# Optimization experiments

Measured on AMD Instinct MI355X. Metric: run time of the kernel, lower is better.

The kernel has to match this reference:

```python
import jax, jax.numpy as jnp
import numpy as np

# dims: S samples, J u-functions, D outputs, P input dims, N data points
S, J, D, P, N = 8, 4, 4, 3, 1024
BG, BU, MG, MU = 32, 32, 10, 32  # g-RFF, u-RFF, g-inducing, u-inducing


def setup_inputs() -> dict:
    key = jax.random.key(0)
    ks = jax.random.split(key, 16)
    ts = jax.random.normal(ks[0], (N, P), dtype=jnp.float32)
    alphas = jax.random.uniform(ks[1], (D, P), minval=0.5, maxval=1.5)   # filter window precisions
    pgs = jax.random.uniform(ks[2], (D, P), minval=0.5, maxval=1.5)      # g kernel precisions (ls2pr)
    zgs = jnp.tile(jnp.linspace(-1.0, 1.0, MG, dtype=jnp.float32)[:, None], (1, P))  # g inducing inputs
    thetag = 2.0 * jax.random.normal(ks[3], (D, P, BG))                  # g spectral freqs
    betag = jax.random.uniform(ks[4], (S, D, P, BG), minval=0.0, maxval=2 * np.pi)
    wg = jax.random.normal(ks[5], (S, D, P, BG)) / np.sqrt(BG)           # g RFF weights
    qg = 0.1 * jax.random.normal(ks[6], (S, D, P, MG))                   # g canonical weights (compute_q)
    pus = jax.random.uniform(ks[7], (P,), minval=0.5, maxval=1.5)        # u cross-kernel precisions
    zus = jax.random.normal(ks[8], (MU, P))                              # u inducing inputs
    thetau = 2.0 * jax.random.normal(ks[9], (S, J, P, BU))               # u spectral freqs
    betau = jax.random.uniform(ks[10], (S, J, BU), minval=0.0, maxval=2 * np.pi)
    wu = jax.random.normal(ks[11], (S, J, BU)) / np.sqrt(BU)
    qu = 0.1 * jax.random.normal(ks[12], (S, J, MU))                     # u canonical weights
    ampu = jnp.float32(1.0)
    log_amps = 0.1 * jax.random.normal(ks[13], (D, J))
    W = jax.random.normal(ks[14], (P, D)) / np.sqrt(P)
    return dict(ts=ts, alphas=alphas, pgs=pgs, zgs=zgs, thetag=thetag, betag=betag,
                wg=wg, qg=qg, pus=pus, zus=zus, thetau=thetau, betau=betau,
                wu=wu, qu=qu, ampu=ampu, log_amps=log_amps, W=W)


def reference(ts, alphas, pgs, zgs, thetag, betag, wg, qg, pus, zus,
              thetau, betau, wu, qu, ampu, log_amps, W):
    """NPGPLayer.forward: f_d(t) = sum_j amps[d,j] * I_dj(t) + ts @ W, where
    I_dj(t) = ampu * int_{R^P} [prod_p exp(-alpha_dp tau_p^2) g_dp(tau_p)] u_j(t - tau) dtau,
    with g, u sampled via random-Fourier + canonical (inducing) features; all 1-D
    Gaussian x cosine integrals are closed-form (this is the math of integrals.full_I)."""
    pi = jnp.pi
    amps = jnp.exp(log_amps)  # [D,J]

    # ---------- Part A: u RFF terms.  Fourier transform of windowed g at om ----------
    om = thetau  # [S,J,P,BU]
    aE = alphas[None, None, :, :, None, None]            # [1,1,D,P,1,1]
    th = thetag[None, None, :, :, None, :]               # [1,1,D,P,1,BG]
    omE = om[:, :, None, :, :, None]                     # [S,J,1,P,BU,1]
    e1 = jnp.exp(-(th - omE) ** 2 / (4 * aE))
    e2 = jnp.exp(-(th + omE) ** 2 / (4 * aE))
    cb = jnp.cos(betag)[:, None, :, :, None, :]
    sb = jnp.sin(betag)[:, None, :, :, None, :]
    wgE = wg[:, None, :, :, None, :]
    # int exp(-a tau^2) cos(th tau + b) e^{-i om tau} dtau
    Ghat_rff = jnp.sum(0.5 * jnp.sqrt(pi / aE) * wgE * ((e1 + e2) * cb + 1j * (e1 - e2) * sb), axis=-1)  # [S,J,D,P,BU]

    A = alphas + pgs                                     # [D,P]
    zT = zgs.T                                           # [P,MG]
    mu = pgs[:, :, None] * zT[None] / A[:, :, None]      # [D,P,MG]
    rg = alphas[:, :, None] * pgs[:, :, None] * zT[None] ** 2 / A[:, :, None]
    decay = jnp.exp(-om[:, :, None, :, :] ** 2 / (4 * A[None, None, :, :, None]))        # [S,J,D,P,BU]
    phase_mu = jnp.exp(-1j * om[:, :, None, :, :, None] * mu[None, None, :, :, None, :])  # [S,J,D,P,BU,MG]
    can_coef = jnp.sqrt(pi / A)[..., None] * jnp.exp(-rg)                                 # [D,P,MG]
    Ghat_can = jnp.sum(qg[:, None, :, :, None, :] * can_coef[None, None, :, :, None, :] * phase_mu, axis=-1) * decay
    Ghat = Ghat_rff + Ghat_can                           # [S,J,D,P,BU] complex

    phase_t = jnp.exp(1j * om[..., None] * ts.T[None, None, :, None, :])  # [S,J,P,BU,N]
    combined = Ghat[..., None] * phase_t[:, :, None]     # [S,J,D,P,BU,N]
    prodp = jnp.prod(combined, axis=3)                   # [S,J,D,BU,N]  (product over input dims)
    cu = wu * jnp.exp(1j * betau)                        # [S,J,BU]
    F_rff = jnp.real(jnp.einsum('sjb,sjdbn->sjdn', cu, prodp))

    # ---------- Part B: u canonical (inducing) terms -- Gaussian x Gaussian integrals ----------
    c = jnp.transpose(ts[:, None, :] - zus[None, :, :], (2, 0, 1))  # [P,N,MU]
    Bm = alphas + pus[None, :]                           # [D,P]
    mp = pus[None, :, None, None] * c[None] / Bm[:, :, None, None]                 # [D,P,N,MU]
    rp = alphas[:, :, None, None] * pus[None, :, None, None] * c[None] ** 2 / Bm[:, :, None, None]
    spec = jnp.sqrt(pi / Bm)[:, :, None] * jnp.exp(-thetag ** 2 / (4 * Bm[:, :, None]))  # [D,P,BG]
    arg = thetag[:, :, None, None, :] * mp[..., None]    # [D,P,N,MU,BG]
    cosx, sinx = jnp.cos(arg), jnp.sin(arg)
    coef1 = wg * jnp.cos(betag) * spec[None]             # [S,D,P,BG]
    coef2 = wg * jnp.sin(betag) * spec[None]
    term_rff = (jnp.einsum('dpnmb,sdpb->sdpnm', cosx, coef1)
                - jnp.einsum('dpnmb,sdpb->sdpnm', sinx, coef2)) * jnp.exp(-rp)[None]
    Cm = Bm + pgs                                        # [D,P]
    diff = mp[..., None] - zT[None, :, None, None, :]    # [D,P,N,MU,MG]
    r2 = Bm[:, :, None, None, None] * pgs[:, :, None, None, None] * diff ** 2 / Cm[:, :, None, None, None]
    val = jnp.sqrt(pi / Cm)[:, :, None, None, None] * jnp.exp(-rp[..., None] - r2)
    term_can = jnp.einsum('dpnmg,sdpg->sdpnm', val, qg)
    Gg = term_rff + term_can                             # [S,D,P,N,MU]
    prodg = jnp.prod(Gg, axis=2)                         # [S,D,N,MU]
    F_can = jnp.einsum('sjm,sdnm->sjdn', qu, prodg)

    F = ampu * (F_rff + F_can)                           # [S,J,D,N]
    layer = jnp.einsum('dj,sjdn->snd', amps, F)          # amps-weighted sum over u functions
    return layer + ts @ W                                # residual connection (is_final_layer=False)
```

## Files before the change

kernel.cpp:

```cpp
#include <hip/hip_runtime.h>
#include <math.h>

#define S_ 8
#define J_ 4
#define D_ 4
#define P_ 3
#define N_ 1024
#define BG_ 32
#define BU_ 32
#define MG_ 10
#define MU_ 32

static constexpr float PI_F = 3.14159265358979323846f;

#define COEF_OFF    0
#define CANPART_OFF 8192

#define NB_CAN  1024
#define NB_COEF 64

__global__ __launch_bounds__(256, 4) void fused_kernel(
    const float* __restrict__ ts,     const float* __restrict__ alphas,
    const float* __restrict__ pgs,    const float* __restrict__ zgs,
    const float* __restrict__ thetag, const float* __restrict__ betag,
    const float* __restrict__ wg,     const float* __restrict__ qg,
    const float* __restrict__ pus,    const float* __restrict__ zus,
    const float* __restrict__ thetau, const float* __restrict__ betau,
    const float* __restrict__ wu,     const float* __restrict__ qu,
    const float* __restrict__ ampu_p, const float* __restrict__ log_amps,
    float* __restrict__ ws)
{
    int bid = blockIdx.x;
    int t   = threadIdx.x;
    float ampu = ampu_p[0];

    if (bid < NB_CAN) {
        __shared__ float sc1[P_][BG_][S_];
        __shared__ float sc2[P_][BG_][S_];
        __shared__ float sqg[P_][MG_][S_];
        __shared__ float stg[P_][BG_];
        __shared__ float szg[P_][MG_];
        __shared__ float szu[P_][MU_];
        __shared__ float sts[4][P_];
        __shared__ float squ[S_][MU_];
        __shared__ float skmp[P_], skrp[P_], sksc[P_], skbc[P_];

        int d  = bid >> 8;
        int n0 = (bid & 255) * 4;

        for (int i = t; i < P_*BG_*S_; i += 256) {
            int p = i >> 8, b = (i >> 3) & 31, s = i & 7;
            float alpha = alphas[d*P_ + p];
            float Bm = alpha + pus[p];
            float th = thetag[(d*P_ + p)*BG_ + b];
            float spec = sqrtf(PI_F / Bm) * __expf(-th*th*0.25f/Bm);
            float be = betag[((s*D_ + d)*P_ + p)*BG_ + b];
            float w  = wg   [((s*D_ + d)*P_ + p)*BG_ + b];
            float sb, cb; __sincosf(be, &sb, &cb);
            sc1[p][b][s] = w * cb * spec;
            sc2[p][b][s] = w * sb * spec;
        }
        for (int i = t; i < P_*MG_*S_; i += 256) {
            int p = i / (MG_*S_), r = i % (MG_*S_), g = r >> 3, s = r & 7;
            ((float*)sqg)[i] = qg[((s*D_ + d)*P_ + p)*MG_ + g];
        }
        {
            int s = t >> 5, m = t & 31;
            float acc = 0.f;
            #pragma unroll
            for (int j = 0; j < J_; ++j)
                acc += __expf(log_amps[d*J_ + j]) * qu[(s*J_ + j)*MU_ + m];
            squ[s][m] = ampu * acc;
        }
        if (t < P_*BG_) ((float*)stg)[t] = thetag[d*P_*BG_ + t];
        if (t < P_*MG_) { int p = t / MG_, g = t % MG_; szg[p][g] = zgs[g*P_ + p]; }
        if (t >= 128 && t < 128 + P_*MU_) {
            int i = t - 128; int p = i >> 5, m = i & 31;
            szu[p][m] = zus[m*P_ + p];
        }
        if (t >= 96 && t < 96 + 4*P_) { int i = t - 96; sts[i/3][i%3] = ts[n0*P_ + i]; }
        if (t >= 112 && t < 112 + P_) {
            int p = t - 112;
            float alpha = alphas[d*P_ + p], pg = pgs[d*P_ + p], pu = pus[p];
            float Bm = alpha + pu, invB = 1.f / Bm;
            skmp[p] = pu * invB;
            skrp[p] = alpha * pu * invB;
            float Cm = Bm + pg, invC = 1.f / Cm;
            sksc[p] = sqrtf(PI_F * invC);
            skbc[p] = Bm * pg * invC;
        }
        __syncthreads();

        int m = t & 31, q = (t >> 5) & 1, nl = t >> 6;

        float pr0=1.f,pr1=1.f,pr2=1.f,pr3=1.f,pr4=1.f,pr5=1.f,pr6=1.f,pr7=1.f;

        #pragma unroll 1
        for (int p = 0; p < P_; ++p) {
            float c  = sts[nl][p] - szu[p][m];
            float mp = skmp[p] * c;
            float E  = __expf(-skrp[p] * c * c);
            float a0=0.f,a1=0.f,a2=0.f,a3=0.f,a4=0.f,a5=0.f,a6=0.f,a7=0.f;
            int b0 = q * 16;
            #pragma unroll 4
            for (int bb = 0; bb < 16; ++bb) {
                int b = b0 + bb;
                float sx, cx; __sincosf(stg[p][b] * mp, &sx, &cx);
                const float4* c1v = (const float4*)&sc1[p][b][0];
                const float4* c2v = (const float4*)&sc2[p][b][0];
                float4 u0 = c1v[0], u1 = c1v[1];
                float4 v0 = c2v[0], v1 = c2v[1];
                a0 += u0.x*cx - v0.x*sx;  a1 += u0.y*cx - v0.y*sx;
                a2 += u0.z*cx - v0.z*sx;  a3 += u0.w*cx - v0.w*sx;
                a4 += u1.x*cx - v1.x*sx;  a5 += u1.y*cx - v1.y*sx;
                a6 += u1.z*cx - v1.z*sx;  a7 += u1.w*cx - v1.w*sx;
            }
            int g0 = q * 5;
            #pragma unroll 1
            for (int gg = 0; gg < 5; ++gg) {
                int g = g0 + gg;
                float diff = mp - szg[p][g];
                float v = sksc[p] * __expf(-skbc[p]*diff*diff);
                const float4* qv = (const float4*)&sqg[p][g][0];
                float4 q0 = qv[0], q1 = qv[1];
                a0 += q0.x*v; a1 += q0.y*v; a2 += q0.z*v; a3 += q0.w*v;
                a4 += q1.x*v; a5 += q1.y*v; a6 += q1.z*v; a7 += q1.w*v;
            }
            a0 += __shfl_xor(a0, 32, 64); a1 += __shfl_xor(a1, 32, 64);
            a2 += __shfl_xor(a2, 32, 64); a3 += __shfl_xor(a3, 32, 64);
            a4 += __shfl_xor(a4, 32, 64); a5 += __shfl_xor(a5, 32, 64);
            a6 += __shfl_xor(a6, 32, 64); a7 += __shfl_xor(a7, 32, 64);
            pr0 *= E*a0; pr1 *= E*a1; pr2 *= E*a2; pr3 *= E*a3;
            pr4 *= E*a4; pr5 *= E*a5; pr6 *= E*a6; pr7 *= E*a7;
        }

        int n = n0 + nl;
        float prod[S_] = {pr0,pr1,pr2,pr3,pr4,pr5,pr6,pr7};
        int s0 = q * 4;
        #pragma unroll
        for (int ss = 0; ss < 4; ++ss) {
            int s = s0 + ss;
            float val = squ[s][m] * prod[s];
            #pragma unroll
            for (int off = 16; off; off >>= 1) val += __shfl_xor(val, off, 32);
            if (m == 0) ws[CANPART_OFF + (s*N_ + n)*D_ + d] = val;
        }
    } else {
        int gtid = (bid - NB_CAN) * 256 + t;
        int q  = gtid & 3;
        int bu = (gtid >> 2) & 31;
        int d  = (gtid >> 7) & 3;
        int j  = (gtid >> 9) & 3;
        int s  = gtid >> 11;
        float G3r = 1.f, G3i = 0.f;
        #pragma unroll 1
        for (int p = 0; p < P_; ++p) {
            float alpha = alphas[d*P_ + p], pg = pgs[d*P_ + p];
            float om    = thetau[((s*J_ + j)*P_ + p)*BU_ + bu];
            float inv4a = 0.25f / alpha;
            float pref  = 0.5f * sqrtf(PI_F / alpha);
            float gr = 0.f, gi = 0.f;
            int b0 = q * 8;
            #pragma unroll 2
            for (int bb = 0; bb < 8; ++bb) {
                int b = b0 + bb;
                float th = thetag[(d*P_ + p)*BG_ + b];
                float dm = th - om, dpl = th + om;
                float e1 = __expf(-dm*dm*inv4a);
                float e2 = __expf(-dpl*dpl*inv4a);
                float be = betag[((s*D_ + d)*P_ + p)*BG_ + b];
                float w  = wg   [((s*D_ + d)*P_ + p)*BG_ + b];
                float sb, cb; __sincosf(be, &sb, &cb);
                gr += pref * w * (e1 + e2) * cb;
                gi += pref * w * (e1 - e2) * sb;
            }
            float A = alpha + pg, invA = 1.f / A;
            float decay = __expf(-om*om*0.25f*invA);
            float cc    = sqrtf(PI_F * invA);
            float cr = 0.f, ci = 0.f;
            int g0 = q * 3, gn = (q < 3) ? 3 : 1;
            #pragma unroll 1
            for (int gg = 0; gg < gn; ++gg) {
                int g = g0 + gg;
                float z  = zgs[g*P_ + p];
                float mu = pg * z * invA;
                float rg = alpha * pg * z * z * invA;
                float cg = cc * __expf(-rg);
                float qv = qg[((s*D_ + d)*P_ + p)*MG_ + g];
                float sm, cm; __sincosf(om * mu, &sm, &cm);
                cr += qv * cg * cm;
                ci -= qv * cg * sm;
            }
            #pragma unroll
            for (int off = 1; off < 4; off <<= 1) {
                gr += __shfl_xor(gr, off, 4);
                gi += __shfl_xor(gi, off, 4);
                cr += __shfl_xor(cr, off, 4);
                ci += __shfl_xor(ci, off, 4);
            }
            float Gr = gr + decay * cr;
            float Gi = gi + decay * ci;
            float nr = G3r*Gr - G3i*Gi;
            float ni = G3r*Gi + G3i*Gr;
            G3r = nr; G3i = ni;
        }
        if (q == 0) {
            float bv = betau[(s*J_ + j)*BU_ + bu];
            float wv = wu   [(s*J_ + j)*BU_ + bu];
            float sbu, cbu; __sincosf(bv, &sbu, &cbu);
            float cuR = wv * cbu, cuI = wv * sbu;
            float amp = ampu * __expf(log_amps[d*J_ + j]);
            int base = (((s*J_ + j)*BU_ + bu)*D_ + d) * 2;
            ws[COEF_OFF + base    ] = amp * (cuR*G3r - cuI*G3i);
            ws[COEF_OFF + base + 1] = amp * (cuR*G3i + cuI*G3r);
        }
    }
}

__global__ __launch_bounds__(256, 4) void final_kernel(
    const float* __restrict__ ts, const float* __restrict__ thetau,
    const float* __restrict__ W,  const float* __restrict__ ws,
    float* __restrict__ out)
{
    __shared__ float sth[J_][P_][BU_];
    __shared__ float scf[J_*BU_][8];
    __shared__ float sW[P_][D_];

    int bid = blockIdx.x;
    int s  = bid >> 7;
    int n0 = (bid & 127) * 8;
    int t  = threadIdx.x;

    for (int i = t; i < J_*P_*BU_; i += 256) ((float*)sth)[i] = thetau[s*J_*P_*BU_ + i];
    for (int i = t; i < J_*BU_*8; i += 256)  ((float*)scf)[i] = ws[COEF_OFF + s*J_*BU_*8 + i];
    if (t < P_*D_) ((float*)sW)[t] = W[t];
    __syncthreads();

    int k = t & 31, nl = t >> 5;
    int n = n0 + nl;
    float t0 = ts[n*P_], t1 = ts[n*P_ + 1], t2 = ts[n*P_ + 2];

    float r0=0.f, r1=0.f, r2=0.f, r3=0.f;
    #pragma unroll 2
    for (int j = 0; j < J_; ++j) {
        float phi = sth[j][0][k]*t0 + sth[j][1][k]*t1 + sth[j][2][k]*t2;
        float sp, cp; __sincosf(phi, &sp, &cp);
        const float4* cfv = (const float4*)&scf[j*BU_ + k][0];
        float4 u = cfv[0], v = cfv[1];
        r0 += u.x*cp - u.y*sp;
        r1 += u.z*cp - u.w*sp;
        r2 += v.x*cp - v.y*sp;
        r3 += v.z*cp - v.w*sp;
    }
    #pragma unroll
    for (int off = 16; off; off >>= 1) {
        r0 += __shfl_xor(r0, off, 32);
        r1 += __shfl_xor(r1, off, 32);
        r2 += __shfl_xor(r2, off, 32);
        r3 += __shfl_xor(r3, off, 32);
    }
    if (k == 0) {
        const float4 cpart = *(const float4*)(ws + CANPART_OFF + (s*N_ + n)*D_);
        float4 o;
        o.x = cpart.x + r0 + t0*sW[0][0] + t1*sW[1][0] + t2*sW[2][0];
        o.y = cpart.y + r1 + t0*sW[0][1] + t1*sW[1][1] + t2*sW[2][1];
        o.z = cpart.z + r2 + t0*sW[0][2] + t1*sW[1][2] + t2*sW[2][2];
        o.w = cpart.w + r3 + t0*sW[0][3] + t1*sW[1][3] + t2*sW[2][3];
        *(float4*)(out + (s*N_ + n)*D_) = o;
    }
}

extern "C" void kernel_launch(void* const* d_in, const int* in_sizes, int n_in,
                              void* d_out, int out_size, void* d_ws, size_t ws_size,
                              hipStream_t stream)
{
    const float* ts       = (const float*)d_in[0];
    const float* alphas   = (const float*)d_in[1];
    const float* pgs      = (const float*)d_in[2];
    const float* zgs      = (const float*)d_in[3];
    const float* thetag   = (const float*)d_in[4];
    const float* betag    = (const float*)d_in[5];
    const float* wg       = (const float*)d_in[6];
    const float* qg       = (const float*)d_in[7];
    const float* pus      = (const float*)d_in[8];
    const float* zus      = (const float*)d_in[9];
    const float* thetau   = (const float*)d_in[10];
    const float* betau    = (const float*)d_in[11];
    const float* wu       = (const float*)d_in[12];
    const float* qu       = (const float*)d_in[13];
    const float* ampu     = (const float*)d_in[14];
    const float* log_amps = (const float*)d_in[15];
    const float* W        = (const float*)d_in[16];
    float* ws  = (float*)d_ws;
    float* out = (float*)d_out;

    fused_kernel<<<NB_CAN + NB_COEF, 256, 0, stream>>>(
        ts, alphas, pgs, zgs, thetag, betag, wg, qg,
        pus, zus, thetau, betau, wu, qu, ampu, log_amps, ws);
    final_kernel<<<1024, 256, 0, stream>>>(ts, thetau, W, ws, out);
}
```

Measured before the change: 27.08 us.

## Process two data points per thread in canonical blocks and schedule coef blocks first

Each canonical block now handles 8 data points instead of 4, with every thread computing two points so the shared-memory coefficient loads (sc1/sc2/sqg) and the per-block setup are amortized over twice the work, halving the canonical block count. The coefficient blocks are moved to the front of the grid so the longer-running coef work starts early instead of trailing. The cost is roughly double the accumulator registers per thread, which may lower occupancy under the launch bounds, and fewer blocks in total.

```diff
diff --git a/kernel.cpp b/kernel.cpp
--- a/kernel.cpp
+++ b/kernel.cpp
@@ -16,8 +16,8 @@
 #define COEF_OFF    0
 #define CANPART_OFF 8192
 
-#define NB_CAN  1024
 #define NB_COEF 64
+#define NB_CAN  512
 
 __global__ __launch_bounds__(256, 4) void fused_kernel(
     const float* __restrict__ ts,     const float* __restrict__ alphas,
@@ -34,19 +34,20 @@
     int t   = threadIdx.x;
     float ampu = ampu_p[0];
 
-    if (bid < NB_CAN) {
+    if (bid >= NB_COEF) {
         __shared__ float sc1[P_][BG_][S_];
         __shared__ float sc2[P_][BG_][S_];
         __shared__ float sqg[P_][MG_][S_];
         __shared__ float stg[P_][BG_];
         __shared__ float szg[P_][MG_];
         __shared__ float szu[P_][MU_];
-        __shared__ float sts[4][P_];
+        __shared__ float sts[8][P_];
         __shared__ float squ[S_][MU_];
         __shared__ float skmp[P_], skrp[P_], sksc[P_], skbc[P_];
 
-        int d  = bid >> 8;
-        int n0 = (bid & 255) * 4;
+        int cb = bid - NB_COEF;
+        int d  = cb >> 7;
+        int n0 = (cb & 127) * 8;
 
         for (int i = t; i < P_*BG_*S_; i += 256) {
             int p = i >> 8, b = (i >> 3) & 31, s = i & 7;
@@ -56,8 +57,8 @@
             float spec = sqrtf(PI_F / Bm) * __expf(-th*th*0.25f/Bm);
             float be = betag[((s*D_ + d)*P_ + p)*BG_ + b];
             float w  = wg   [((s*D_ + d)*P_ + p)*BG_ + b];
-            float sb, cb; __sincosf(be, &sb, &cb);
-            sc1[p][b][s] = w * cb * spec;
+            float sb, cbv; __sincosf(be, &sb, &cbv);
+            sc1[p][b][s] = w * cbv * spec;
             sc2[p][b][s] = w * sb * spec;
         }
         for (int i = t; i < P_*MG_*S_; i += 256) {
@@ -78,9 +79,9 @@
             int i = t - 128; int p = i >> 5, m = i & 31;
             szu[p][m] = zus[m*P_ + p];
         }
-        if (t >= 96 && t < 96 + 4*P_) { int i = t - 96; sts[i/3][i%3] = ts[n0*P_ + i]; }
-        if (t >= 112 && t < 112 + P_) {
-            int p = t - 112;
+        if (t >= 96 && t < 96 + 8*P_) { int i = t - 96; sts[i/3][i%3] = ts[n0*P_ + i]; }
+        if (t >= 120 && t < 120 + P_) {
+            int p = t - 120;
             float alpha = alphas[d*P_ + p], pg = pgs[d*P_ + p], pu = pus[p];
             float Bm = alpha + pu, invB = 1.f / Bm;
             skmp[p] = pu * invB;
@@ -92,61 +93,94 @@
         __syncthreads();
 
         int m = t & 31, q = (t >> 5) & 1, nl = t >> 6;
-
-        float pr0=1.f,pr1=1.f,pr2=1.f,pr3=1.f,pr4=1.f,pr5=1.f,pr6=1.f,pr7=1.f;
+        int rA = nl*2, rB = nl*2 + 1;
+
+        float pA0=1.f,pA1=1.f,pA2=1.f,pA3=1.f,pA4=1.f,pA5=1.f,pA6=1.f,pA7=1.f;
+        float pB0=1.f,pB1=1.f,pB2=1.f,pB3=1.f,pB4=1.f,pB5=1.f,pB6=1.f,pB7=1.f;
 
         #pragma unroll 1
         for (int p = 0; p < P_; ++p) {
-            float c  = sts[nl][p] - szu[p][m];
-            float mp = skmp[p] * c;
-            float E  = __expf(-skrp[p] * c * c);
-            float a0=0.f,a1=0.f,a2=0.f,a3=0.f,a4=0.f,a5=0.f,a6=0.f,a7=0.f;
+            float zu = szu[p][m];
+            float cA = sts[rA][p] - zu;
+            float cB = sts[rB][p] - zu;
+            float mpA = skmp[p] * cA, mpB = skmp[p] * cB;
+            float EA = __expf(-skrp[p] * cA * cA);
+            float EB = __expf(-skrp[p] * cB * cB);
+
+            float aA0=0.f,aA1=0.f,aA2=0.f,aA3=0.f,aA4=0.f,aA5=0.f,aA6=0.f,aA7=0.f;
+            float aB0=0.f,aB1=0.f,aB2=0.f,aB3=0.f,aB4=0.f,aB5=0.f,aB6=0.f,aB7=0.f;
+
             int b0 = q * 16;
-            #pragma unroll 4
+            #pragma unroll 2
             for (int bb = 0; bb < 16; ++bb) {
                 int b = b0 + bb;
-                float sx, cx; __sincosf(stg[p][b] * mp, &sx, &cx);
+                float th = stg[p][b];
+                float sxA, cxA; __sincosf(th * mpA, &sxA, &cxA);
+                float sxB, cxB; __sincosf(th * mpB, &sxB, &cxB);
                 const float4* c1v = (const float4*)&sc1[p][b][0];
                 const float4* c2v = (const float4*)&sc2[p][b][0];
                 float4 u0 = c1v[0], u1 = c1v[1];
                 float4 v0 = c2v[0], v1 = c2v[1];
-                a0 += u0.x*cx - v0.x*sx;  a1 += u0.y*cx - v0.y*sx;
-                a2 += u0.z*cx - v0.z*sx;  a3 += u0.w*cx - v0.w*sx;
-                a4 += u1.x*cx - v1.x*sx;  a5 += u1.y*cx - v1.y*sx;
-                a6 += u1.z*cx - v1.z*sx;  a7 += u1.w*cx - v1.w*sx;
+                aA0 += u0.x*cxA - v0.x*sxA;  aA1 += u0.y*cxA - v0.y*sxA;
+                aA2 += u0.z*cxA - v0.z*sxA;  aA3 += u0.w*cxA - v0.w*sxA;
+                aA4 += u1.x*cxA - v1.x*sxA;  aA5 += u1.y*cxA - v1.y*sxA;
+                aA6 += u1.z*cxA - v1.z*sxA;  aA7 += u1.w*cxA - v1.w*sxA;
+                aB0 += u0.x*cxB - v0.x*sxB;  aB1 += u0.y*cxB - v0.y*sxB;
+                aB2 += u0.z*cxB - v0.z*sxB;  aB3 += u0.w*cxB - v0.w*sxB;
+                aB4 += u1.x*cxB - v1.x*sxB;  aB5 += u1.y*cxB - v1.y*sxB;
+                aB6 += u1.z*cxB - v1.z*sxB;  aB7 += u1.w*cxB - v1.w*sxB;
             }
             int g0 = q * 5;
             #pragma unroll 1
             for (int gg = 0; gg < 5; ++gg) {
                 int g = g0 + gg;
-                float diff = mp - szg[p][g];
-                float v = sksc[p] * __expf(-skbc[p]*diff*diff);
+                float zg = szg[p][g];
+                float dA = mpA - zg, dB = mpB - zg;
+                float vA = sksc[p] * __expf(-skbc[p]*dA*dA);
+                float vB = sksc[p] * __expf(-skbc[p]*dB*dB);
                 const float4* qv = (const float4*)&sqg[p][g][0];
                 float4 q0 = qv[0], q1 = qv[1];
-                a0 += q0.x*v; a1 += q0.y*v; a2 += q0.z*v; a3 += q0.w*v;
-                a4 += q1.x*v; a5 += q1.y*v; a6 += q1.z*v; a7 += q1.w*v;
-            }
-            a0 += __shfl_xor(a0, 32, 64); a1 += __shfl_xor(a1, 32, 64);
-            a2 += __shfl_xor(a2, 32, 64); a3 += __shfl_xor(a3, 32, 64);
-            a4 += __shfl_xor(a4, 32, 64); a5 += __shfl_xor(a5, 32, 64);
-            a6 += __shfl_xor(a6, 32, 64); a7 += __shfl_xor(a7, 32, 64);
-            pr0 *= E*a0; pr1 *= E*a1; pr2 *= E*a2; pr3 *= E*a3;
-            pr4 *= E*a4; pr5 *= E*a5; pr6 *= E*a6; pr7 *= E*a7;
-        }
-
-        int n = n0 + nl;
-        float prod[S_] = {pr0,pr1,pr2,pr3,pr4,pr5,pr6,pr7};
+                aA0 += q0.x*vA; aA1 += q0.y*vA; aA2 += q0.z*vA; aA3 += q0.w*vA;
+                aA4 += q1.x*vA; aA5 += q1.y*vA; aA6 += q1.z*vA; aA7 += q1.w*vA;
+                aB0 += q0.x*vB; aB1 += q0.y*vB; aB2 += q0.z*vB; aB3 += q0.w*vB;
+                aB4 += q1.x*vB; aB5 += q1.y*vB; aB6 += q1.z*vB; aB7 += q1.w*vB;
+            }
+            aA0 += __shfl_xor(aA0, 32, 64); aA1 += __shfl_xor(aA1, 32, 64);
+            aA2 += __shfl_xor(aA2, 32, 64); aA3 += __shfl_xor(aA3, 32, 64);
+            aA4 += __shfl_xor(aA4, 32, 64); aA5 += __shfl_xor(aA5, 32, 64);
+            aA6 += __shfl_xor(aA6, 32, 64); aA7 += __shfl_xor(aA7, 32, 64);
+            aB0 += __shfl_xor(aB0, 32, 64); aB1 += __shfl_xor(aB1, 32, 64);
+            aB2 += __shfl_xor(aB2, 32, 64); aB3 += __shfl_xor(aB3, 32, 64);
+            aB4 += __shfl_xor(aB4, 32, 64); aB5 += __shfl_xor(aB5, 32, 64);
+            aB6 += __shfl_xor(aB6, 32, 64); aB7 += __shfl_xor(aB7, 32, 64);
+            pA0 *= EA*aA0; pA1 *= EA*aA1; pA2 *= EA*aA2; pA3 *= EA*aA3;
+            pA4 *= EA*aA4; pA5 *= EA*aA5; pA6 *= EA*aA6; pA7 *= EA*aA7;
+            pB0 *= EB*aB0; pB1 *= EB*aB1; pB2 *= EB*aB2; pB3 *= EB*aB3;
+            pB4 *= EB*aB4; pB5 *= EB*aB5; pB6 *= EB*aB6; pB7 *= EB*aB7;
+        }
+
+        float prodA[S_] = {pA0,pA1,pA2,pA3,pA4,pA5,pA6,pA7};
+        float prodB[S_] = {pB0,pB1,pB2,pB3,pB4,pB5,pB6,pB7};
+        int nA = n0 + rA, nB = n0 + rB;
         int s0 = q * 4;
         #pragma unroll
         for (int ss = 0; ss < 4; ++ss) {
-            int s = s0 + ss;
-            float val = squ[s][m] * prod[s];
+            int s = ss + s0;
+            float qu_sm = squ[s][m];
+            float vA = qu_sm * prodA[s];
+            float vB = qu_sm * prodB[s];
             #pragma unroll
-            for (int off = 16; off; off >>= 1) val += __shfl_xor(val, off, 32);
-            if (m == 0) ws[CANPART_OFF + (s*N_ + n)*D_ + d] = val;
+            for (int off = 16; off; off >>= 1) {
+                vA += __shfl_xor(vA, off, 32);
+                vB += __shfl_xor(vB, off, 32);
+            }
+            if (m == 0) {
+                ws[CANPART_OFF + (s*N_ + nA)*D_ + d] = vA;
+                ws[CANPART_OFF + (s*N_ + nB)*D_ + d] = vB;
+            }
         }
     } else {
-        int gtid = (bid - NB_CAN) * 256 + t;
+        int gtid = bid * 256 + t;
         int q  = gtid & 3;
         int bu = (gtid >> 2) & 31;
         int d  = (gtid >> 7) & 3;
@@ -294,7 +328,7 @@
     float* ws  = (float*)d_ws;
     float* out = (float*)d_out;
 
-    fused_kernel<<<NB_CAN + NB_COEF, 256, 0, stream>>>(
+    fused_kernel<<<NB_COEF + NB_CAN, 256, 0, stream>>>(
         ts, alphas, pgs, zgs, thetag, betag, wg, qg,
         pus, zus, thetau, betau, wu, qu, ampu, log_amps, ws);
     final_kernel<<<1024, 256, 0, stream>>>(ts, thetau, W, ws, out);
```

Result: faster. 26.04 us (median of 2 runs) (-3.8%).
